# Kernel optimization log

Measured on AMD Instinct MI355X. Metric: run time of the kernel, lower is better.

Reference implementation:

```python
import jax, jax.numpy as jnp
import numpy as np

B, S, D = 4, 2048, 2048
H, K = 16, 128          # num_heads, intermediate_dim
FINAL = H * K           # 2048
VDIM = 2048             # vector_dim
EPS_LN = 1e-6
EPS_NORM = 1e-30


def setup_inputs() -> dict:
    key = jax.random.key(0)
    ks = jax.random.split(key, 8)
    x = jax.random.normal(ks[0], (B, S, D), dtype=jnp.float32)
    vector = jax.random.normal(ks[1], (B, VDIM), dtype=jnp.float32)
    W_att = jax.random.normal(ks[2], (D, H), dtype=jnp.float32) / np.sqrt(D)
    temperature = jnp.ones((1, 1, H), dtype=jnp.float32)
    W_values = jax.random.normal(ks[3], (D, H, K), dtype=jnp.float32) / np.sqrt(D)
    W_op = jax.random.normal(ks[4], (FINAL, VDIM), dtype=jnp.float32) / np.sqrt(FINAL)
    ff1 = jax.random.normal(ks[5], (VDIM + D, D), dtype=jnp.float32) / np.sqrt(VDIM + D)
    ff1_b = jnp.zeros((1, 1, D), dtype=jnp.float32)
    ff2 = jax.random.normal(ks[6], (D, D), dtype=jnp.float32) / np.sqrt(D)
    ff2_b = jnp.zeros((1, 1, D), dtype=jnp.float32)
    gamma = jnp.ones((D,), dtype=jnp.float32)
    beta = jnp.zeros((D,), dtype=jnp.float32)
    return {"x": x, "vector": vector, "W_att": W_att, "temperature": temperature,
            "W_values": W_values, "W_op": W_op, "ff1": ff1, "ff1_b": ff1_b,
            "ff2": ff2, "ff2_b": ff2_b, "gamma": gamma, "beta": beta}


def reference(x, vector, W_att, temperature, W_values, W_op, ff1, ff1_b, ff2, ff2_b, gamma, beta):
    b, s, d = x.shape
    # attention gate per (query) position -- [B,S,H]
    logits = jnp.matmul(x, W_att)
    logits = logits - jnp.max(logits, axis=-2, keepdims=True)
    w = jnp.exp(logits * temperature)
    # exact collapse of repeat+tril+normalize: A[b,i,j,h] = w[b,i,h]*tril[i,j]
    # denom[b,i,h] = w[b,i,h]*(i+1) + 1e-30  ->  out = coef * causal cumsum of v
    counts = jnp.arange(1, s + 1, dtype=x.dtype)[None, :, None]  # [1,S,1]
    coef = w / (w * counts + EPS_NORM)                            # [B,S,H]
    v = jnp.einsum('bsi,ihk->bshk', x, W_values)                  # [B,S,H,K]
    cum_v = jnp.cumsum(v, axis=1)                                 # prefix-sum over keys
    pooled = (coef[..., None] * cum_v).reshape(b, s, -1)          # [B,S,H*K]
    op = jnp.matmul(pooled, W_op) + vector[:, None, :]            # [B,S,VDIM]
    concat = jnp.concatenate([x, op], axis=-1)                    # [B,S,VDIM+D]
    h = jax.nn.relu(jnp.matmul(concat, ff1) + ff1_b)
    h = jax.nn.relu(jnp.matmul(h, ff2) + ff2_b)
    res = h + x
    mean = jnp.mean(res, axis=-1, keepdims=True)
    cen = res - mean
    var = jnp.mean(cen * cen, axis=-1, keepdims=True)
    return cen / jnp.sqrt(var + EPS_LN) * gamma + beta
```

## Files before the change

kernel.cpp:

```cpp
#include <hip/hip_runtime.h>
#include <stdint.h>

#define B_DIM 4
#define S_DIM 2048
#define D_DIM 2048
#define H_DIM 16
#define M_ROWS (B_DIM * S_DIM)
#define CONCAT_LD 4096
#define NCHUNK 32
#define CHLEN (S_DIM / NCHUNK)

#define BM 128
#define BN 128
#define BK 64

typedef __attribute__((ext_vector_type(8))) __bf16 bf16x8;
typedef __attribute__((ext_vector_type(4))) float f32x4;

__device__ inline unsigned short f2bf(float f) {
  union { float f; unsigned u; } x; x.f = f;
  unsigned r = x.u + 0x7fffu + ((x.u >> 16) & 1u);
  return (unsigned short)(r >> 16);
}
__device__ inline float bf2f(unsigned short s) {
  union { unsigned u; float f; } x; x.u = ((unsigned)s) << 16;
  return x.f;
}

__global__ __launch_bounds__(256) void xconv_logits_kernel(
    const float* __restrict__ x, const float* __restrict__ Watt,
    unsigned short* __restrict__ concat, float* __restrict__ logits) {
  int row = blockIdx.x, t = threadIdx.x;
  const float* xr = x + (size_t)row * D_DIM;
  unsigned short* cr = concat + (size_t)row * CONCAT_LD;
  float p[H_DIM];
#pragma unroll
  for (int h = 0; h < H_DIM; ++h) p[h] = 0.f;
#pragma unroll
  for (int i = 0; i < 8; ++i) {
    int k = t + i * 256;
    float xv = xr[k];
    cr[k] = f2bf(xv);
    const float* wr = Watt + (size_t)k * H_DIM;
#pragma unroll
    for (int h = 0; h < H_DIM; ++h) p[h] += xv * wr[h];
  }
  __shared__ float red[4][H_DIM];
  int l = t & 63, w = t >> 6;
#pragma unroll
  for (int h = 0; h < H_DIM; ++h) {
    float v = p[h];
    for (int off = 32; off; off >>= 1) v += __shfl_down(v, off);
    if (l == 0) red[w][h] = v;
  }
  __syncthreads();
  if (t < H_DIM)
    logits[(size_t)row * H_DIM + t] = red[0][t] + red[1][t] + red[2][t] + red[3][t];
}

__global__ __launch_bounds__(256) void transpose_conv_kernel(
    const float* __restrict__ src, unsigned short* __restrict__ dst,
    int R, int C, int ldd) {
  __shared__ float tile[32][33];
  int c0 = blockIdx.x * 32, r0 = blockIdx.y * 32;
  int tx = threadIdx.x & 31, ty = threadIdx.x >> 5;
#pragma unroll
  for (int i = 0; i < 32; i += 8)
    tile[ty + i][tx] = src[(size_t)(r0 + ty + i) * C + c0 + tx];
  __syncthreads();
#pragma unroll
  for (int i = 0; i < 32; i += 8)
    dst[(size_t)(c0 + ty + i) * ldd + r0 + tx] = f2bf(tile[tx][ty + i]);
}

__global__ __launch_bounds__(256) void convert_kernel(
    const float* __restrict__ src, unsigned short* __restrict__ dst) {
  int idx = (blockIdx.x * 256 + threadIdx.x) * 4;
  const float4 v = *(const float4*)(src + idx);
  ushort4 o;
  o.x = f2bf(v.x); o.y = f2bf(v.y); o.z = f2bf(v.z); o.w = f2bf(v.w);
  *(ushort4*)(dst + idx) = o;
}

__global__ __launch_bounds__(256) void coef_kernel(
    const float* __restrict__ logits, const float* __restrict__ temp, float* __restrict__ coef) {
  int b = blockIdx.x >> 4, h = blockIdx.x & 15;
  int t = threadIdx.x;
  const float* lg = logits + (size_t)b * S_DIM * H_DIM + h;
  float mx = -1e30f;
  for (int s = t; s < S_DIM; s += 256) mx = fmaxf(mx, lg[(size_t)s * H_DIM]);
  for (int off = 32; off; off >>= 1) mx = fmaxf(mx, __shfl_down(mx, off));
  __shared__ float red[4];
  if ((t & 63) == 0) red[t >> 6] = mx;
  __syncthreads();
  mx = fmaxf(fmaxf(red[0], red[1]), fmaxf(red[2], red[3]));
  float T = temp[h];
  float* cf = coef + (size_t)b * S_DIM * H_DIM + h;
  for (int s = t; s < S_DIM; s += 256) {
    float w = expf((lg[(size_t)s * H_DIM] - mx) * T);
    cf[(size_t)s * H_DIM] = w / (w * (float)(s + 1) + 1e-30f);
  }
}

__global__ __launch_bounds__(256) void bias2_partial_kernel(
    const float* __restrict__ vector, const float* __restrict__ ff1,
    float* __restrict__ part) {
  int n = blockIdx.x * 256 + threadIdx.x;
  int seg = blockIdx.y, b = blockIdx.z;
  const float* vr = vector + (size_t)b * 2048 + seg * 128;
  const float* fr = ff1 + (size_t)(2048 + seg * 128) * 2048 + n;
  float acc = 0.f;
#pragma unroll 8
  for (int j = 0; j < 128; ++j) acc += vr[j] * fr[(size_t)j * 2048];
  part[((size_t)seg * 4 + b) * 2048 + n] = acc;
}

__global__ __launch_bounds__(256) void bias2_reduce_kernel(
    const float* __restrict__ part, const float* __restrict__ ff1_b,
    float* __restrict__ bias2) {
  int n = blockIdx.x * 256 + threadIdx.x;
  int b = blockIdx.y;
  float acc = ff1_b[n];
#pragma unroll
  for (int s = 0; s < 16; ++s) acc += part[((size_t)s * 4 + b) * 2048 + n];
  bias2[(size_t)b * 2048 + n] = acc;
}

template <int MODE>
__global__ __launch_bounds__(256) void gemm_bt_kernel(
    const unsigned short* __restrict__ A, int lda,
    const unsigned short* __restrict__ Bt, int ldb, int K,
    void* __restrict__ outp, int ldo,
    const float* __restrict__ bias, const float* __restrict__ resid) {
  __shared__ unsigned short As[BM * BK];
  __shared__ unsigned short Bs[BN * BK];
  const int t = threadIdx.x;
  const int w = t >> 6, l = t & 63;
  const int wm = w & 1, wn = w >> 1;
  const int q = l >> 4, ln = l & 15;

  const int L = blockIdx.y * 16 + blockIdx.x;
  const int xcd = L & 7;
  const int W = L >> 3;
  const int bx = W & 15;
  const int by = (W >> 4) * 8 + xcd;
  const int m0 = by * BM, n0 = bx * BN;

  f32x4 acc[4][4];
#pragma unroll
  for (int i = 0; i < 4; ++i)
#pragma unroll
    for (int j = 0; j < 4; ++j) acc[i][j] = {0.f, 0.f, 0.f, 0.f};

  for (int k0 = 0; k0 < K; k0 += BK) {
    __syncthreads();
#pragma unroll
    for (int r = 0; r < 4; ++r) {
      int s = r * 256 + t;
      int row = s >> 3;
      int ch = (s & 7) ^ (row & 7);
      const unsigned short* ga = A + (size_t)(m0 + row) * lda + k0 + ch * 8;
      __builtin_amdgcn_global_load_lds(
          (const __attribute__((address_space(1))) void*)ga,
          (__attribute__((address_space(3))) void*)(As + (r * 256 + w * 64) * 8), 16, 0, 0);
      const unsigned short* gb = Bt + (size_t)(n0 + row) * ldb + k0 + ch * 8;
      __builtin_amdgcn_global_load_lds(
          (const __attribute__((address_space(1))) void*)gb,
          (__attribute__((address_space(3))) void*)(Bs + (r * 256 + w * 64) * 8), 16, 0, 0);
    }
    __syncthreads();
#pragma unroll
    for (int h = 0; h < 2; ++h) {
      bf16x8 af[4], bfr[4];
#pragma unroll
      for (int mt = 0; mt < 4; ++mt) {
        int ar = wm * 64 + mt * 16 + ln;
        af[mt] = *(const bf16x8*)&As[ar * BK + (((h * 4 + q) ^ (ar & 7)) * 8)];
      }
#pragma unroll
      for (int nt = 0; nt < 4; ++nt) {
        int br = wn * 64 + nt * 16 + ln;
        bfr[nt] = *(const bf16x8*)&Bs[br * BK + (((h * 4 + q) ^ (br & 7)) * 8)];
      }
#pragma unroll
      for (int mt = 0; mt < 4; ++mt)
#pragma unroll
        for (int nt = 0; nt < 4; ++nt)
          acc[mt][nt] = __builtin_amdgcn_mfma_f32_16x16x32_bf16(af[mt], bfr[nt], acc[mt][nt], 0, 0, 0);
    }
  }

#pragma unroll
  for (int mt = 0; mt < 4; ++mt) {
#pragma unroll
    for (int i = 0; i < 4; ++i) {
      int row = m0 + wm * 64 + mt * 16 + q * 4 + i;
#pragma unroll
      for (int nt = 0; nt < 4; ++nt) {
        int col = n0 + wn * 64 + nt * 16 + ln;
        float vv = acc[mt][nt][i];
        if (MODE == 2) { vv += bias[(size_t)(row >> 11) * 2048 + col]; vv = fmaxf(vv, 0.f); }
        if (MODE == 4) {
          vv += bias[col]; vv = fmaxf(vv, 0.f);
          vv += resid[(size_t)row * 2048 + col];
          ((float*)outp)[(size_t)row * ldo + col] = vv;
        } else {
          ((unsigned short*)outp)[(size_t)row * ldo + col] = f2bf(vv);
        }
      }
    }
  }
}

#define GLD16(g, s)                                                        \
  __builtin_amdgcn_global_load_lds(                                        \
      (const __attribute__((address_space(1))) void*)(g),                  \
      (__attribute__((address_space(3))) void*)(s), 16, 0, 0)
#define BARX() asm volatile("s_barrier" ::: "memory")
#define VMW6() asm volatile("s_waitcnt vmcnt(6)" ::: "memory")
#define VMW4() asm volatile("s_waitcnt vmcnt(4)" ::: "memory")
#define VMW0() asm volatile("s_waitcnt vmcnt(0)" ::: "memory")

#define LD_A4(areg, base, buf, h)                                          \
  do {                                                                     \
    _Pragma("unroll") for (int _i = 0; _i < 4; ++_i) {                     \
      int ar = wm * 128 + ((base) + _i) * 16 + ln;                         \
      areg[(base) + _i] = *(const bf16x8*)&As[buf][h][ar * 32 + rsel];     \
    }                                                                      \
  } while (0)

#define LD_B2(breg, buf, h, np)                                            \
  do {                                                                     \
    _Pragma("unroll") for (int _i = 0; _i < 2; ++_i) {                     \
      int br = wn * 64 + ((np)*2 + _i) * 16 + ln;                          \
      breg[_i] = *(const bf16x8*)&Bs[buf][h][br * 32 + rsel];              \
    }                                                                      \
  } while (0)

#define MM(areg, breg, np)                                                 \
  do {                                                                     \
    __builtin_amdgcn_s_setprio(1);                                         \
    _Pragma("unroll") for (int _mt = 0; _mt < 8; ++_mt) {                  \
      _Pragma("unroll") for (int _i = 0; _i < 2; ++_i)                     \
          acc[_mt][(np)*2 + _i] = __builtin_amdgcn_mfma_f32_16x16x32_bf16( \
              areg[_mt], breg[_i], acc[_mt][(np)*2 + _i], 0, 0, 0);        \
    }                                                                      \
    __builtin_amdgcn_s_setprio(0);                                         \
  } while (0)

template <int MODE>
__global__ __launch_bounds__(512, 2) void gemm256_kernel(
    const unsigned short* __restrict__ A, int lda,
    const unsigned short* __restrict__ Bt, int ldb, int K,
    void* __restrict__ outp, int ldo,
    const float* __restrict__ bias, const float* __restrict__ resid) {
  __shared__ unsigned short As[2][2][256 * 32];
  __shared__ unsigned short Bs[2][2][256 * 32];
  const int t = threadIdx.x;
  const int wv = t >> 6, l = t & 63;
  const int wm = wv >> 2, wn = wv & 3;
  const int q = l >> 4, ln = l & 15;

  const int L = blockIdx.y * 8 + blockIdx.x;
  const int lin = (L & 7) * 32 + (L >> 3);
  const int m0 = (lin >> 3) * 256, n0 = (lin & 7) * 256;

  const int srow = t >> 2;
  const int scol = (((t & 3) * 16) ^ (((srow >> 1) & 3) << 4)) >> 1;
  const unsigned short* Abase = A + (size_t)(m0 + srow) * lda + scol;
  const unsigned short* Bbase = Bt + (size_t)(n0 + srow) * ldb + scol;
  const size_t astep = (size_t)128 * lda, bstep = (size_t)128 * ldb;
  const int rsel = (q * 8) ^ (((ln >> 1) & 3) << 3);

  f32x4 acc[8][4];
#pragma unroll
  for (int i = 0; i < 8; ++i)
#pragma unroll
    for (int j = 0; j < 4; ++j) acc[i][j] = {0.f, 0.f, 0.f, 0.f};

  auto stageA = [&](int kt, int kh, int buf) {
    const unsigned short* g = Abase + (size_t)kt * 64 + kh * 32;
    GLD16(g, &As[buf][kh][wv * 512]);
    GLD16(g + astep, &As[buf][kh][4096 + wv * 512]);
  };
  auto stageB = [&](int kt, int kh, int buf) {
    const unsigned short* g = Bbase + (size_t)kt * 64 + kh * 32;
    GLD16(g, &Bs[buf][kh][wv * 512]);
    GLD16(g + bstep, &Bs[buf][kh][4096 + wv * 512]);
  };

  bf16x8 a0[8], a1[8], ba[2], bb[2];

  const int NT = K >> 6;
  stageA(0, 0, 0); stageB(0, 0, 0);
  stageA(0, 1, 0); stageB(0, 1, 0);
  stageA(1, 0, 1); stageB(1, 0, 1);
  VMW4();
  BARX();
  LD_A4(a0, 0, 0, 0);
  LD_A4(a0, 4, 0, 0);
  LD_B2(ba, 0, 0, 0);

  for (int tt = 0; tt < NT; ++tt) {
    const int c = tt & 1;
    const int t1 = (tt + 1 == NT) ? 0 : tt + 1;
    const int t2 = (tt + 2 >= NT) ? tt + 2 - NT : tt + 2;
    LD_B2(bb, c, 0, 1);
    LD_A4(a1, 0, c, 1);
    stageA(t1, 1, c ^ 1);
    BARX();
    MM(a0, ba, 0);
    VMW6();
    BARX();
    LD_A4(a1, 4, c, 1);
    LD_B2(ba, c, 1, 0);
    stageB(t1, 1, c ^ 1);
    BARX();
    MM(a0, bb, 1);
    VMW6();
    BARX();
    LD_B2(bb, c, 1, 1);
    LD_A4(a0, 0, c ^ 1, 0);
    stageA(t2, 0, c);
    BARX();
    MM(a1, ba, 0);
    VMW6();
    BARX();
    LD_A4(a0, 4, c ^ 1, 0);
    LD_B2(ba, c ^ 1, 0, 0);
    stageB(t2, 0, c);
    BARX();
    MM(a1, bb, 1);
    VMW6();
    BARX();
  }
  VMW0();

#pragma unroll
  for (int mt = 0; mt < 8; ++mt) {
#pragma unroll
    for (int i = 0; i < 4; ++i) {
      int row = m0 + wm * 128 + mt * 16 + q * 4 + i;
#pragma unroll
      for (int nt = 0; nt < 4; ++nt) {
        int col = n0 + wn * 64 + nt * 16 + ln;
        float vv = acc[mt][nt][i];
        if (MODE == 2) { vv += bias[(size_t)(row >> 11) * 2048 + col]; vv = fmaxf(vv, 0.f); }
        if (MODE == 4) {
          vv += bias[col]; vv = fmaxf(vv, 0.f);
          vv += resid[(size_t)row * 2048 + col];
          ((float*)outp)[(size_t)row * ldo + col] = vv;
        } else {
          ((unsigned short*)outp)[(size_t)row * ldo + col] = f2bf(vv);
        }
      }
    }
  }
}

__global__ __launch_bounds__(256) void scan_partial_kernel(
    const unsigned short* __restrict__ v, float* __restrict__ csum) {
  int c = blockIdx.x * 256 + threadIdx.x;
  int chunk = blockIdx.y, b = blockIdx.z;
  const unsigned short* p = v + ((size_t)(b * S_DIM + chunk * CHLEN)) * D_DIM + c;
  float s = 0.f;
#pragma unroll 4
  for (int i = 0; i < CHLEN; ++i) s += bf2f(p[(size_t)i * D_DIM]);
  csum[((size_t)b * NCHUNK + chunk) * D_DIM + c] = s;
}

__global__ __launch_bounds__(256) void scan_offsets_kernel(float* __restrict__ csum) {
  int c = blockIdx.x * 256 + threadIdx.x;
  int b = blockIdx.y;
  float run = 0.f;
  float* p = csum + (size_t)b * NCHUNK * D_DIM + c;
  for (int ch = 0; ch < NCHUNK; ++ch) {
    float tv = p[(size_t)ch * D_DIM];
    p[(size_t)ch * D_DIM] = run;
    run += tv;
  }
}

__global__ __launch_bounds__(256) void scan_apply_kernel(
    const unsigned short* __restrict__ v, const float* __restrict__ csum,
    const float* __restrict__ coef, unsigned short* __restrict__ pooled_out) {
  int c = blockIdx.x * 256 + threadIdx.x;
  int chunk = blockIdx.y, b = blockIdx.z;
  int h = c >> 7;
  int row0 = b * S_DIM + chunk * CHLEN;
  float run = csum[((size_t)b * NCHUNK + chunk) * D_DIM + c];
  const unsigned short* vp = v + (size_t)row0 * D_DIM + c;
  unsigned short* po = pooled_out + (size_t)row0 * CONCAT_LD + c;
  const float* cf = coef + (size_t)row0 * H_DIM + h;
#pragma unroll 4
  for (int i = 0; i < CHLEN; ++i) {
    run += bf2f(vp[(size_t)i * D_DIM]);
    po[(size_t)i * CONCAT_LD] = f2bf(cf[(size_t)i * H_DIM] * run);
  }
}

__global__ __launch_bounds__(256) void ln_kernel(
    float* __restrict__ out, const float* __restrict__ gamma, const float* __restrict__ beta) {
  int row = blockIdx.x, t = threadIdx.x;
  float* pr = out + (size_t)row * D_DIM;
  float vals[8];
  float s = 0.f;
#pragma unroll
  for (int i = 0; i < 8; ++i) { vals[i] = pr[t + i * 256]; s += vals[i]; }
  __shared__ float red[4];
  for (int off = 32; off; off >>= 1) s += __shfl_down(s, off);
  if ((t & 63) == 0) red[t >> 6] = s;
  __syncthreads();
  float mean = (red[0] + red[1] + red[2] + red[3]) * (1.f / D_DIM);
  __syncthreads();
  float c2 = 0.f;
#pragma unroll
  for (int i = 0; i < 8; ++i) { float c = vals[i] - mean; c2 += c * c; }
  for (int off = 32; off; off >>= 1) c2 += __shfl_down(c2, off);
  if ((t & 63) == 0) red[t >> 6] = c2;
  __syncthreads();
  float var = (red[0] + red[1] + red[2] + red[3]) * (1.f / D_DIM);
  float rstd = rsqrtf(var + 1e-6f);
#pragma unroll
  for (int i = 0; i < 8; ++i) {
    int col = t + i * 256;
    pr[col] = (vals[i] - mean) * rstd * gamma[col] + beta[col];
  }
}

extern "C" void kernel_launch(void* const* d_in, const int* in_sizes, int n_in,
                              void* d_out, int out_size, void* d_ws, size_t ws_size,
                              hipStream_t stream) {
  const float* x      = (const float*)d_in[0];
  const float* vector = (const float*)d_in[1];
  const float* W_att  = (const float*)d_in[2];
  const float* temp   = (const float*)d_in[3];
  const float* W_val  = (const float*)d_in[4];
  const float* W_op   = (const float*)d_in[5];
  const float* ff1    = (const float*)d_in[6];
  const float* ff1_b  = (const float*)d_in[7];
  const float* ff2    = (const float*)d_in[8];
  const float* ff2_b  = (const float*)d_in[9];
  const float* gamma  = (const float*)d_in[10];
  const float* beta   = (const float*)d_in[11];
  float* out = (float*)d_out;

  char* ws = (char*)d_ws;
  auto alloc = [&](size_t bytes) {
    char* p = ws; ws += (bytes + 255) & ~(size_t)255; return p;
  };
  unsigned short* concat = (unsigned short*)alloc((size_t)M_ROWS * CONCAT_LD * 2);
  unsigned short* wv_t   = (unsigned short*)alloc((size_t)2048 * 2048 * 2);
  unsigned short* btff1  = (unsigned short*)alloc((size_t)2048 * 4096 * 2);
  unsigned short* f1bT   = (unsigned short*)alloc((size_t)2048 * 2048 * 2);
  unsigned short* wop_bf = (unsigned short*)alloc((size_t)2048 * 2048 * 2);
  unsigned short* ff2_t  = (unsigned short*)alloc((size_t)2048 * 2048 * 2);
  unsigned short* vbuf   = (unsigned short*)alloc((size_t)M_ROWS * 2048 * 2);
  unsigned short* h1     = (unsigned short*)alloc((size_t)M_ROWS * 2048 * 2);
  float* logits = (float*)alloc((size_t)M_ROWS * H_DIM * 4);
  float* coef   = (float*)alloc((size_t)M_ROWS * H_DIM * 4);
  float* csum   = (float*)alloc((size_t)B_DIM * NCHUNK * D_DIM * 4);
  float* part   = (float*)alloc((size_t)16 * 4 * 2048 * 4);
  float* bias2  = (float*)alloc((size_t)4 * 2048 * 4);

  xconv_logits_kernel<<<M_ROWS, 256, 0, stream>>>(x, W_att, concat, logits);
  transpose_conv_kernel<<<dim3(64, 64), 256, 0, stream>>>(W_val, wv_t, 2048, 2048, 2048);
  transpose_conv_kernel<<<dim3(64, 64), 256, 0, stream>>>(ff1, btff1, 2048, 2048, 4096);
  transpose_conv_kernel<<<dim3(64, 64), 256, 0, stream>>>(ff1 + (size_t)2048 * 2048, f1bT, 2048, 2048, 2048);
  convert_kernel<<<2048 * 2048 / 1024, 256, 0, stream>>>(W_op, wop_bf);
  transpose_conv_kernel<<<dim3(64, 64), 256, 0, stream>>>(ff2, ff2_t, 2048, 2048, 2048);
  coef_kernel<<<B_DIM * H_DIM, 256, 0, stream>>>(logits, temp, coef);
  gemm_bt_kernel<1><<<dim3(16, 16), 256, 0, stream>>>(
      f1bT, 2048, wop_bf, 2048, 2048, btff1 + 2048, 4096, nullptr, nullptr);
  bias2_partial_kernel<<<dim3(8, 16, 4), 256, 0, stream>>>(vector, ff1, part);
  bias2_reduce_kernel<<<dim3(8, 4), 256, 0, stream>>>(part, ff1_b, bias2);
  gemm256_kernel<1><<<dim3(8, 32), 512, 0, stream>>>(
      concat, CONCAT_LD, wv_t, 2048, 2048, vbuf, 2048, nullptr, nullptr);
  scan_partial_kernel<<<dim3(8, NCHUNK, B_DIM), 256, 0, stream>>>(vbuf, csum);
  scan_offsets_kernel<<<dim3(8, B_DIM), 256, 0, stream>>>(csum);
  scan_apply_kernel<<<dim3(8, NCHUNK, B_DIM), 256, 0, stream>>>(vbuf, csum, coef, concat + 2048);
  gemm256_kernel<2><<<dim3(8, 32), 512, 0, stream>>>(
      concat, CONCAT_LD, btff1, 4096, 4096, h1, 2048, bias2, nullptr);
  gemm256_kernel<4><<<dim3(8, 32), 512, 0, stream>>>(
      h1, 2048, ff2_t, 2048, 2048, out, 2048, ff2_b, x);
  ln_kernel<<<M_ROWS, 256, 0, stream>>>(out, gamma, beta);
}
```

Baseline: 718.4 us.

## Merge weight prep kernels, fold scan offsets into apply, restructure GEMM register schedule

The four weight transposes and the W_op conversion now run as one launch, selected by blockIdx.z. The separate scan-offsets kernel is removed, and each scan_apply block instead sums the preceding chunk totals itself. The 256-tile GEMM inner loop is rescheduled to load 4 B fragments and 4 A fragments at a time and issue a 4x4 MFMA block per step, with extra barriers and no cross-iteration register prefetch. This cuts launches and register pressure, but the new GEMM schedule exposes more LDS latency and adds barriers.

```diff
diff --git a/kernel.cpp b/kernel.cpp
--- a/kernel.cpp
+++ b/kernel.cpp
@@ -58,28 +58,38 @@
     logits[(size_t)row * H_DIM + t] = red[0][t] + red[1][t] + red[2][t] + red[3][t];
 }
 
-__global__ __launch_bounds__(256) void transpose_conv_kernel(
-    const float* __restrict__ src, unsigned short* __restrict__ dst,
-    int R, int C, int ldd) {
+__global__ __launch_bounds__(256) void prep_kernel(
+    const float* __restrict__ Wval, const float* __restrict__ ff1,
+    const float* __restrict__ ff2, const float* __restrict__ Wop,
+    unsigned short* __restrict__ wv_t, unsigned short* __restrict__ btff1,
+    unsigned short* __restrict__ f1bT, unsigned short* __restrict__ ff2_t,
+    unsigned short* __restrict__ wop_bf) {
+  int z = blockIdx.z;
+  if (z == 4) {
+    size_t idx = (((size_t)blockIdx.y * 64 + blockIdx.x) * 256 + threadIdx.x) * 4;
+    const float4 v = *(const float4*)(Wop + idx);
+    ushort4 o;
+    o.x = f2bf(v.x); o.y = f2bf(v.y); o.z = f2bf(v.z); o.w = f2bf(v.w);
+    *(ushort4*)(wop_bf + idx) = o;
+    return;
+  }
+  const float* src;
+  unsigned short* dst;
+  int ldd;
+  if (z == 0)      { src = Wval;                        dst = wv_t;  ldd = 2048; }
+  else if (z == 1) { src = ff1;                         dst = btff1; ldd = 4096; }
+  else if (z == 2) { src = ff1 + (size_t)2048 * 2048;   dst = f1bT;  ldd = 2048; }
+  else             { src = ff2;                         dst = ff2_t; ldd = 2048; }
   __shared__ float tile[32][33];
   int c0 = blockIdx.x * 32, r0 = blockIdx.y * 32;
   int tx = threadIdx.x & 31, ty = threadIdx.x >> 5;
 #pragma unroll
   for (int i = 0; i < 32; i += 8)
-    tile[ty + i][tx] = src[(size_t)(r0 + ty + i) * C + c0 + tx];
+    tile[ty + i][tx] = src[(size_t)(r0 + ty + i) * 2048 + c0 + tx];
   __syncthreads();
 #pragma unroll
   for (int i = 0; i < 32; i += 8)
     dst[(size_t)(c0 + ty + i) * ldd + r0 + tx] = f2bf(tile[tx][ty + i]);
-}
-
-__global__ __launch_bounds__(256) void convert_kernel(
-    const float* __restrict__ src, unsigned short* __restrict__ dst) {
-  int idx = (blockIdx.x * 256 + threadIdx.x) * 4;
-  const float4 v = *(const float4*)(src + idx);
-  ushort4 o;
-  o.x = f2bf(v.x); o.y = f2bf(v.y); o.z = f2bf(v.z); o.w = f2bf(v.w);
-  *(ushort4*)(dst + idx) = o;
 }
 
 __global__ __launch_bounds__(256) void coef_kernel(
@@ -221,29 +231,29 @@
 #define VMW4() asm volatile("s_waitcnt vmcnt(4)" ::: "memory")
 #define VMW0() asm volatile("s_waitcnt vmcnt(0)" ::: "memory")
 
-#define LD_A4(areg, base, buf, h)                                          \
+#define LD_A4(areg, buf, h, mbase)                                         \
   do {                                                                     \
     _Pragma("unroll") for (int _i = 0; _i < 4; ++_i) {                     \
-      int ar = wm * 128 + ((base) + _i) * 16 + ln;                         \
-      areg[(base) + _i] = *(const bf16x8*)&As[buf][h][ar * 32 + rsel];     \
+      int ar = wm * 128 + ((mbase) + _i) * 16 + ln;                        \
+      areg[_i] = *(const bf16x8*)&As[buf][h][ar * 32 + rsel];              \
     }                                                                      \
   } while (0)
 
-#define LD_B2(breg, buf, h, np)                                            \
+#define LD_B4(buf, h)                                                      \
   do {                                                                     \
-    _Pragma("unroll") for (int _i = 0; _i < 2; ++_i) {                     \
-      int br = wn * 64 + ((np)*2 + _i) * 16 + ln;                          \
-      breg[_i] = *(const bf16x8*)&Bs[buf][h][br * 32 + rsel];              \
+    _Pragma("unroll") for (int _i = 0; _i < 4; ++_i) {                     \
+      int br = wn * 64 + _i * 16 + ln;                                     \
+      bk[_i] = *(const bf16x8*)&Bs[buf][h][br * 32 + rsel];                \
     }                                                                      \
   } while (0)
 
-#define MM(areg, breg, np)                                                 \
+#define MMR(areg, rowbase)                                                 \
   do {                                                                     \
     __builtin_amdgcn_s_setprio(1);                                         \
-    _Pragma("unroll") for (int _mt = 0; _mt < 8; ++_mt) {                  \
-      _Pragma("unroll") for (int _i = 0; _i < 2; ++_i)                     \
-          acc[_mt][(np)*2 + _i] = __builtin_amdgcn_mfma_f32_16x16x32_bf16( \
-              areg[_mt], breg[_i], acc[_mt][(np)*2 + _i], 0, 0, 0);        \
+    _Pragma("unroll") for (int _j = 0; _j < 4; ++_j) {                     \
+      _Pragma("unroll") for (int _n = 0; _n < 4; ++_n)                     \
+          acc[(rowbase) + _j][_n] = __builtin_amdgcn_mfma_f32_16x16x32_bf16( \
+              areg[_j], bk[_n], acc[(rowbase) + _j][_n], 0, 0, 0);         \
     }                                                                      \
     __builtin_amdgcn_s_setprio(0);                                         \
   } while (0)
@@ -289,7 +299,7 @@
     GLD16(g + bstep, &Bs[buf][kh][4096 + wv * 512]);
   };
 
-  bf16x8 a0[8], a1[8], ba[2], bb[2];
+  bf16x8 aL[4], aH[4], bk[4];
 
   const int NT = K >> 6;
   stageA(0, 0, 0); stageB(0, 0, 0);
@@ -297,40 +307,33 @@
   stageA(1, 0, 1); stageB(1, 0, 1);
   VMW4();
   BARX();
-  LD_A4(a0, 0, 0, 0);
-  LD_A4(a0, 4, 0, 0);
-  LD_B2(ba, 0, 0, 0);
 
   for (int tt = 0; tt < NT; ++tt) {
     const int c = tt & 1;
     const int t1 = (tt + 1 == NT) ? 0 : tt + 1;
     const int t2 = (tt + 2 >= NT) ? tt + 2 - NT : tt + 2;
-    LD_B2(bb, c, 0, 1);
-    LD_A4(a1, 0, c, 1);
+    LD_A4(aL, c, 0, 0);
+    LD_B4(c, 0);
     stageA(t1, 1, c ^ 1);
     BARX();
-    MM(a0, ba, 0);
+    MMR(aL, 0);
+    BARX();
+    LD_A4(aH, c, 0, 4);
+    stageB(t1, 1, c ^ 1);
+    BARX();
+    MMR(aH, 4);
     VMW6();
     BARX();
-    LD_A4(a1, 4, c, 1);
-    LD_B2(ba, c, 1, 0);
-    stageB(t1, 1, c ^ 1);
-    BARX();
-    MM(a0, bb, 1);
-    VMW6();
-    BARX();
-    LD_B2(bb, c, 1, 1);
-    LD_A4(a0, 0, c ^ 1, 0);
+    LD_A4(aL, c, 1, 0);
+    LD_B4(c, 1);
     stageA(t2, 0, c);
     BARX();
-    MM(a1, ba, 0);
-    VMW6();
-    BARX();
-    LD_A4(a0, 4, c ^ 1, 0);
-    LD_B2(ba, c ^ 1, 0, 0);
+    MMR(aL, 0);
+    BARX();
+    LD_A4(aH, c, 1, 4);
     stageB(t2, 0, c);
     BARX();
-    MM(a1, bb, 1);
+    MMR(aH, 4);
     VMW6();
     BARX();
   }
@@ -369,18 +372,6 @@
   csum[((size_t)b * NCHUNK + chunk) * D_DIM + c] = s;
 }
 
-__global__ __launch_bounds__(256) void scan_offsets_kernel(float* __restrict__ csum) {
-  int c = blockIdx.x * 256 + threadIdx.x;
-  int b = blockIdx.y;
-  float run = 0.f;
-  float* p = csum + (size_t)b * NCHUNK * D_DIM + c;
-  for (int ch = 0; ch < NCHUNK; ++ch) {
-    float tv = p[(size_t)ch * D_DIM];
-    p[(size_t)ch * D_DIM] = run;
-    run += tv;
-  }
-}
-
 __global__ __launch_bounds__(256) void scan_apply_kernel(
     const unsigned short* __restrict__ v, const float* __restrict__ csum,
     const float* __restrict__ coef, unsigned short* __restrict__ pooled_out) {
@@ -388,7 +379,9 @@
   int chunk = blockIdx.y, b = blockIdx.z;
   int h = c >> 7;
   int row0 = b * S_DIM + chunk * CHLEN;
-  float run = csum[((size_t)b * NCHUNK + chunk) * D_DIM + c];
+  const float* cs = csum + (size_t)b * NCHUNK * D_DIM + c;
+  float run = 0.f;
+  for (int j = 0; j < chunk; ++j) run += cs[(size_t)j * D_DIM];
   const unsigned short* vp = v + (size_t)row0 * D_DIM + c;
   unsigned short* po = pooled_out + (size_t)row0 * CONCAT_LD + c;
   const float* cf = coef + (size_t)row0 * H_DIM + h;
@@ -463,12 +456,9 @@
   float* part   = (float*)alloc((size_t)16 * 4 * 2048 * 4);
   float* bias2  = (float*)alloc((size_t)4 * 2048 * 4);
 
+  prep_kernel<<<dim3(64, 64, 5), 256, 0, stream>>>(
+      W_val, ff1, ff2, W_op, wv_t, btff1, f1bT, ff2_t, wop_bf);
   xconv_logits_kernel<<<M_ROWS, 256, 0, stream>>>(x, W_att, concat, logits);
-  transpose_conv_kernel<<<dim3(64, 64), 256, 0, stream>>>(W_val, wv_t, 2048, 2048, 2048);
-  transpose_conv_kernel<<<dim3(64, 64), 256, 0, stream>>>(ff1, btff1, 2048, 2048, 4096);
-  transpose_conv_kernel<<<dim3(64, 64), 256, 0, stream>>>(ff1 + (size_t)2048 * 2048, f1bT, 2048, 2048, 2048);
-  convert_kernel<<<2048 * 2048 / 1024, 256, 0, stream>>>(W_op, wop_bf);
-  transpose_conv_kernel<<<dim3(64, 64), 256, 0, stream>>>(ff2, ff2_t, 2048, 2048, 2048);
   coef_kernel<<<B_DIM * H_DIM, 256, 0, stream>>>(logits, temp, coef);
   gemm_bt_kernel<1><<<dim3(16, 16), 256, 0, stream>>>(
       f1bT, 2048, wop_bf, 2048, 2048, btff1 + 2048, 4096, nullptr, nullptr);
@@ -477,7 +467,6 @@
   gemm256_kernel<1><<<dim3(8, 32), 512, 0, stream>>>(
       concat, CONCAT_LD, wv_t, 2048, 2048, vbuf, 2048, nullptr, nullptr);
   scan_partial_kernel<<<dim3(8, NCHUNK, B_DIM), 256, 0, stream>>>(vbuf, csum);
-  scan_offsets_kernel<<<dim3(8, B_DIM), 256, 0, stream>>>(csum);
   scan_apply_kernel<<<dim3(8, NCHUNK, B_DIM), 256, 0, stream>>>(vbuf, csum, coef, concat + 2048);
   gemm256_kernel<2><<<dim3(8, 32), 512, 0, stream>>>(
       concat, CONCAT_LD, btff1, 4096, 4096, h1, 2048, bias2, nullptr);
```

New measurement: 718.2 us. No clear change (-0.0%).
